# Kernel tuning notes

Measured on AMD Instinct MI355X. Metric: run time of the kernel, lower is better.

The kernel has to match this reference:

```python
import jax, jax.numpy as jnp
import numpy as np

N = 50000
E = 800000
HIGH, LOW, EMB = 128, 32, 64
HID, HEADS, OUT = 32, 8, 8
IN1 = HIGH + EMB  # 192
IN2 = HID * HEADS  # 256
NEG_SLOPE = 0.2


def setup_inputs() -> dict:
    key = jax.random.key(0)
    ks = jax.random.split(key, 12)
    s = lambda k, shape: (jax.random.normal(k, shape, dtype=jnp.float32) * 0.1)
    return {
        "high_dim_features": jax.random.normal(ks[0], (N, HIGH), dtype=jnp.float32),
        "low_dim_features": jax.random.normal(ks[1], (N, LOW), dtype=jnp.float32),
        "edge_index": jax.random.randint(ks[2], (2, E), 0, N, dtype=jnp.int32),
        "W_emb": s(ks[3], (LOW, EMB)),
        "b_emb": jnp.zeros((EMB,), jnp.float32),
        "W1": s(ks[4], (IN1, HEADS * HID)),
        "att_src1": s(ks[5], (HEADS, HID)),
        "att_dst1": s(ks[6], (HEADS, HID)),
        "b1": jnp.zeros((HEADS * HID,), jnp.float32),
        "W2": s(ks[7], (IN2, OUT)),
        "att_src2": s(ks[8], (1, OUT)),
        "att_dst2": s(ks[9], (1, OUT)),
        "b2": jnp.zeros((OUT,), jnp.float32),
    }


def _gat_layer(x, src, dst, W, att_src, att_dst, bias, heads, out_ch, concat):
    # x: [N, F_in]; src/dst: [E'] (self-loops already appended)
    n = x.shape[0]
    h = (x @ W).reshape(n, heads, out_ch)            # [N, H, C]
    a_src = jnp.einsum('nhc,hc->nh', h, att_src)     # [N, H]
    a_dst = jnp.einsum('nhc,hc->nh', h, att_dst)
    alpha = a_src[src] + a_dst[dst]                  # [E', H]
    alpha = jax.nn.leaky_relu(alpha, NEG_SLOPE)
    # segment softmax over incoming edges per destination node
    m = jax.ops.segment_max(alpha, dst, num_segments=n)
    ea = jnp.exp(alpha - m[dst])
    z = jax.ops.segment_sum(ea, dst, num_segments=n)
    alpha = ea / (z[dst] + 1e-16)                    # [E', H]
    msg = h[src] * alpha[:, :, None]                 # [E', H, C]
    out = jax.ops.segment_sum(msg, dst, num_segments=n)  # [N, H, C]
    if concat:
        out = out.reshape(n, heads * out_ch)
    else:
        out = out.mean(axis=1)
    return out + bias


def reference(high_dim_features, low_dim_features, edge_index,
              W_emb, b_emb, W1, att_src1, att_dst1, b1,
              W2, att_src2, att_dst2, b2):
    # embedding + elu, concat
    emb = jax.nn.elu(low_dim_features @ W_emb + b_emb)
    x = jnp.concatenate([high_dim_features, emb], axis=1)  # [N, IN1]
    # add self-loops (PyG default)
    loops = jnp.arange(N, dtype=edge_index.dtype)
    src = jnp.concatenate([edge_index[0], loops])
    dst = jnp.concatenate([edge_index[1], loops])
    x = _gat_layer(x, src, dst, W1, att_src1, att_dst1, b1, HEADS, HID, True)
    x = jax.nn.elu(x)  # dropout: eval mode no-op
    x = _gat_layer(x, src, dst, W2, att_src2, att_dst2, b2, 1, OUT, False)
    return jax.nn.log_softmax(x, axis=1)
```

## Files before the change

### kernel.cpp

```cpp
#include <hip/hip_runtime.h>
#include <hip/hip_bf16.h>

typedef __hip_bfloat16 bf16;
typedef short bf16x8 __attribute__((ext_vector_type(8)));
typedef float f32x4  __attribute__((ext_vector_type(4)));

#define CHK 8192

__device__ __forceinline__ float bf2f(bf16 v){ return __bfloat162float(v); }
__device__ __forceinline__ bf16  f2bf(float f){ return __float2bfloat16(f); }
__device__ __forceinline__ float lrelu(float a){ return a > 0.f ? a : 0.2f*a; }
__device__ __forceinline__ float bfbits(short s){
    union{unsigned u; float f;} cv; cv.u = ((unsigned)(unsigned short)s) << 16; return cv.f;
}
__device__ __forceinline__ short bf16s(float f){ bf16 q = f2bf(f); return *(short*)&q; }
__device__ __forceinline__ float cvtf(const void* p, int i, int isb){
    return isb ? bf2f(((const bf16*)p)[i]) : ((const float*)p)[i];
}
__device__ __forceinline__ short cvts(const void* p, int i, int isb){
    return isb ? ((const short*)p)[i] : bf16s(((const float*)p)[i]);
}
__device__ __forceinline__ bf16x8 load8(const void* base, size_t off, int isb){
    if (isb) return *(const bf16x8*)((const bf16*)base + off);
    const float* f = (const float*)base + off;
    f32x4 v0 = *(const f32x4*)f;
    f32x4 v1 = *(const f32x4*)(f + 4);
    short r[8];
    #pragma unroll
    for (int j = 0; j < 4; j++) r[j]   = bf16s(v0[j]);
    #pragma unroll
    for (int j = 0; j < 4; j++) r[4+j] = bf16s(v1[j]);
    return *(const bf16x8*)r;
}

__global__ __launch_bounds__(256) void k_init(const unsigned short* __restrict__ raw,
        int* __restrict__ flag, const int* __restrict__ dst,
        int* __restrict__ bucketCnt, int E, int NBUK, int nBlk){
    __shared__ int h[256];
    int t = threadIdx.x;
    if (blockIdx.x == 0){
        unsigned short w = raw[2*t];
        int e = (w >> 7) & 0xFF;
        int ok = (e >= 90 && e <= 140) ? 1 : 0;
        __shared__ int cnt;
        if (t == 0) cnt = 0;
        __syncthreads();
        atomicAdd(&cnt, ok);
        __syncthreads();
        if (t == 0) *flag = (cnt >= 192) ? 1 : 0;
    }
    h[t] = 0;
    __syncthreads();
    for (int i = blockIdx.x*256 + t; i < E; i += nBlk*256)
        atomicAdd(&h[((unsigned)dst[i]) >> 8], 1);
    __syncthreads();
    if (t < NBUK && h[t]) atomicAdd(&bucketCnt[t], h[t]);
}

__global__ __launch_bounds__(256) void k_prep(const void* __restrict__ low,
        const void* __restrict__ Wemb, const void* __restrict__ bemb,
        const void* __restrict__ W1, const void* __restrict__ W2,
        bf16* __restrict__ emb, bf16* __restrict__ Bp, bf16* __restrict__ Bp2,
        const int* __restrict__ flag, int N, int nEmb){
    __shared__ float wem[2048 + 64];
    __shared__ short lows[1024];
    int t = threadIdx.x;
    int b = blockIdx.x;
    int isb = *flag;
    if (b >= nEmb){
        int i = (b - nEmb)*256 + t;
        if (i < 16*6*64*8){
            int j = i & 7;
            int lane = (i >> 3) & 63;
            int r = i >> 9;
            int kt = r % 6, nt = r / 6;
            int k = kt*32 + (lane >> 4)*8 + j;
            int n = nt*16 + (lane & 15);
            *(short*)&Bp[i] = cvts(W1, k*256 + n, isb);
        } else {
            int i2 = i - 16*6*64*8;
            if (i2 >= 8*64*8) return;
            int j = i2 & 7;
            int lane = (i2 >> 3) & 63;
            int kt = i2 >> 9;
            int k = kt*32 + (lane >> 4)*8 + j;
            int n = lane & 15;
            *(short*)&Bp2[i2] = (n < 8) ? cvts(W2, k*8 + n, isb) : (short)0;
        }
        return;
    }
    int nb0 = b * 32;
    for (int i = t; i < 2048; i += 256) wem[i] = cvtf(Wemb, i, isb);
    if (t < 64) wem[2048 + t] = cvtf(bemb, t, isb);
    int lim = (N - nb0) * 32; if (lim > 1024) lim = 1024;
    for (int i = t; i < 1024; i += 256)
        lows[i] = (i < lim) ? cvts(low, nb0*32 + i, isb) : (short)0;
    __syncthreads();
    int nl = t >> 3, j8 = (t & 7) * 8;
    float acc[8];
    #pragma unroll
    for (int j = 0; j < 8; j++) acc[j] = wem[2048 + j8 + j];
    for (int k = 0; k < 32; k++){
        float lv = bfbits(lows[nl*32 + k]);
        f32x4 w0 = *(const f32x4*)&wem[k*64 + j8];
        f32x4 w1 = *(const f32x4*)&wem[k*64 + j8 + 4];
        #pragma unroll
        for (int j = 0; j < 4; j++) acc[j]   += lv * w0[j];
        #pragma unroll
        for (int j = 0; j < 4; j++) acc[4+j] += lv * w1[j];
    }
    int n = nb0 + nl;
    if (n < N){
        short ov[8];
        #pragma unroll
        for (int j = 0; j < 8; j++){
            float v = acc[j];
            ov[j] = bf16s(v > 0.f ? v : expm1f(v));
        }
        *(bf16x8*)&emb[(size_t)n*64 + j8] = *(const bf16x8*)ov;
    }
}

__global__ __launch_bounds__(256) void k_bscan(const int* __restrict__ bucketCnt,
        int* __restrict__ bucketPtr, int* __restrict__ bucketCur,
        int* __restrict__ rowptr, int N, int E, int NBUK){
    __shared__ int sd[256];
    int t = threadIdx.x;
    int v = (t < NBUK) ? bucketCnt[t] : 0;
    sd[t] = v;
    __syncthreads();
    #pragma unroll
    for (int off = 1; off < 256; off <<= 1){
        int a = (t >= off) ? sd[t - off] : 0;
        __syncthreads();
        sd[t] += a;
        __syncthreads();
    }
    int excl = sd[t] - v;
    if (t < NBUK){ bucketPtr[t] = excl; bucketCur[t] = excl; }
    if (t == 0){ bucketPtr[NBUK] = sd[255]; rowptr[N] = E + N; }
}

__global__ __launch_bounds__(256, 3) void k_sg(
        const int* __restrict__ ei, int* __restrict__ bucketCur, int* __restrict__ pk,
        const void* __restrict__ highv, const bf16* __restrict__ emb,
        const bf16* __restrict__ Bp, const void* __restrict__ attS,
        const void* __restrict__ attD, bf16* __restrict__ h1,
        float* __restrict__ a_s, float* __restrict__ a_d,
        const int* __restrict__ flag, int N, int E, int nG, int NBUK){
    const int RS = 260;
    __shared__ union SM {
        struct { float eb[16*260 + 16]; float att[512]; } g;
        struct { unsigned short dstS[CHK]; int hist[256]; int cur[256]; } s;
    } sm;
    int t = threadIdx.x;
    if ((int)blockIdx.x >= nG){
        int cb = blockIdx.x - nG;
        int base = cb * CHK;
        int cnt = E - base; if (cnt > CHK) cnt = CHK;
        sm.s.hist[t] = 0;
        __syncthreads();
        const int* dstp = ei + E + base;
        for (int i = t; i < cnt; i += 256){
            int d = dstp[i];
            sm.s.dstS[i] = (unsigned short)d;
            atomicAdd(&sm.s.hist[((unsigned)d) >> 8], 1);
        }
        __syncthreads();
        if (t < NBUK){
            int c = sm.s.hist[t];
            sm.s.cur[t] = c ? atomicAdd(&bucketCur[t], c) : 0;
        }
        __syncthreads();
        const int* srcp = ei + base;
        for (int i = t; i < cnt; i += 256){
            int d = sm.s.dstS[i];
            int pos = atomicAdd(&sm.s.cur[d >> 8], 1);
            pk[pos] = ((d & 255) << 24) | srcp[i];
        }
        return;
    }
    float* eb  = sm.g.eb;
    float* att = sm.g.att;
    int isb = *flag;
    att[t] = cvtf(attS, t, isb);
    att[256 + t] = cvtf(attD, t, isb);
    int w = t >> 6, lane = t & 63;
    int m_lo = lane & 15, quad = lane >> 4;
    int m0 = blockIdx.x * 64;
    int mr[4];
    #pragma unroll
    for (int rt = 0; rt < 4; rt++){
        int m = m0 + rt*16 + m_lo;
        mr[rt] = m < N ? m : N-1;
    }
    f32x4 acc[4][4];
    #pragma unroll
    for (int rt = 0; rt < 4; rt++)
        #pragma unroll
        for (int ct = 0; ct < 4; ct++) acc[rt][ct] = (f32x4){0.f,0.f,0.f,0.f};

    #pragma unroll 2
    for (int kt = 0; kt < 6; kt++){
        bf16x8 a[4], b[4];
        if (kt < 4){
            #pragma unroll
            for (int rt = 0; rt < 4; rt++)
                a[rt] = load8(highv, (size_t)mr[rt]*128 + kt*32 + quad*8, isb);
        } else {
            #pragma unroll
            for (int rt = 0; rt < 4; rt++)
                a[rt] = *(const bf16x8*)&emb[(size_t)mr[rt]*64 + (kt-4)*32 + quad*8];
        }
        #pragma unroll
        for (int ct = 0; ct < 4; ct++)
            b[ct] = *(const bf16x8*)&Bp[(size_t)(((w*4 + ct)*6 + kt)*64 + lane)*8];
        #pragma unroll
        for (int rt = 0; rt < 4; rt++)
            #pragma unroll
            for (int ct = 0; ct < 4; ct++)
                acc[rt][ct] = __builtin_amdgcn_mfma_f32_16x16x32_bf16(a[rt], b[ct], acc[rt][ct], 0, 0, 0);
    }

    #pragma unroll 1
    for (int rt = 0; rt < 4; rt++){
        __syncthreads();
        #pragma unroll
        for (int ct = 0; ct < 4; ct++)
            #pragma unroll
            for (int reg = 0; reg < 4; reg++)
                eb[(quad*4 + reg)*RS + w*64 + ct*16 + m_lo] = acc[rt][ct][reg];
        __syncthreads();
        int r = t >> 4, cb = t & 15;
        int c0 = cb * 16;
        int m = m0 + rt*16 + r;
        f32x4 v[4];
        #pragma unroll
        for (int p = 0; p < 4; p++) v[p] = *(const f32x4*)&eb[r*RS + c0 + p*4];
        float ps = 0.f, pd = 0.f;
        #pragma unroll
        for (int p = 0; p < 4; p++)
            #pragma unroll
            for (int j = 0; j < 4; j++){
                ps += v[p][j] * att[c0 + p*4 + j];
                pd += v[p][j] * att[256 + c0 + p*4 + j];
            }
        if (m < N){
            short ov[16];
            #pragma unroll
            for (int p = 0; p < 4; p++)
                #pragma unroll
                for (int j = 0; j < 4; j++) ov[p*4+j] = bf16s(v[p][j]);
            *(bf16x8*)&h1[(size_t)m*256 + c0]     = *(const bf16x8*)&ov[0];
            *(bf16x8*)&h1[(size_t)m*256 + c0 + 8] = *(const bf16x8*)&ov[8];
        }
        ps += __shfl_xor(ps, 1);
        pd += __shfl_xor(pd, 1);
        if (((t & 1) == 0) && m < N){
            int hd = cb >> 1;
            a_s[m*8 + hd] = ps;
            a_d[m*8 + hd] = pd;
        }
    }
}

__global__ __launch_bounds__(256) void k_fine(const int* __restrict__ bucketPtr,
        const int* __restrict__ pk, int* __restrict__ rowptr, int* __restrict__ srcs,
        int N){
    __shared__ int cnt[256];
    __shared__ int sd[256];
    int t = threadIdx.x;
    int b = blockIdx.x;
    int d0 = b << 8;
    int nd = N - d0; if (nd > 256) nd = 256;
    int ebeg = bucketPtr[b], eend = bucketPtr[b+1];
    cnt[t] = (t < nd) ? 1 : 0;
    __syncthreads();
    for (int i = ebeg + t; i < eend; i += 256)
        atomicAdd(&cnt[((unsigned)pk[i]) >> 24], 1);
    __syncthreads();
    int v = cnt[t];
    sd[t] = v;
    __syncthreads();
    #pragma unroll
    for (int off = 1; off < 256; off <<= 1){
        int a = (t >= off) ? sd[t - off] : 0;
        __syncthreads();
        sd[t] += a;
        __syncthreads();
    }
    int r = ebeg + d0 + sd[t] - v;
    if (t < nd){
        rowptr[d0 + t] = r;
        srcs[r] = d0 + t;
        cnt[t] = r + 1;
    }
    __syncthreads();
    for (int i = ebeg + t; i < eend; i += 256){
        int p = pk[i];
        int pos = atomicAdd(&cnt[((unsigned)p) >> 24], 1);
        srcs[pos] = p & 0xFFFFFF;
    }
}

__global__ __launch_bounds__(256) void k_edge1(const int* __restrict__ rowptr,
        const int* __restrict__ srcs, const float* __restrict__ a_s,
        const float* __restrict__ a_d, const bf16* __restrict__ h1,
        const void* __restrict__ b1, bf16* __restrict__ x2,
        const int* __restrict__ flag, int N){
    int t = threadIdx.x;
    int lane = t & 63, wv = t >> 6;
    int n = blockIdx.x*4 + wv;
    if (n >= N) return;
    int beg = rowptr[n];
    int deg = rowptr[n+1] - beg;

    int cl = lane & 31;
    int hb = cl >> 2;
    int half = lane >> 5;
    float adb = a_d[n*8 + hb];

    float acc[8];
    #pragma unroll
    for (int j = 0; j < 8; j++) acc[j] = 0.f;
    float z = 0.f;

    int e = half;
    for (; e + 6 < deg; e += 8){
        int s0 = srcs[beg + e];
        int s1 = srcs[beg + e + 2];
        int s2 = srcs[beg + e + 4];
        int s3 = srcs[beg + e + 6];
        float w0 = __expf(fminf(lrelu(a_s[s0*8 + hb] + adb), 80.f));
        float w1 = __expf(fminf(lrelu(a_s[s1*8 + hb] + adb), 80.f));
        float w2 = __expf(fminf(lrelu(a_s[s2*8 + hb] + adb), 80.f));
        float w3 = __expf(fminf(lrelu(a_s[s3*8 + hb] + adb), 80.f));
        bf16x8 v0 = *(const bf16x8*)&h1[(size_t)s0*256 + cl*8];
        bf16x8 v1 = *(const bf16x8*)&h1[(size_t)s1*256 + cl*8];
        bf16x8 v2 = *(const bf16x8*)&h1[(size_t)s2*256 + cl*8];
        bf16x8 v3 = *(const bf16x8*)&h1[(size_t)s3*256 + cl*8];
        z += (w0 + w1) + (w2 + w3);
        #pragma unroll
        for (int j = 0; j < 8; j++) acc[j] += w0 * bfbits(v0[j]);
        #pragma unroll
        for (int j = 0; j < 8; j++) acc[j] += w1 * bfbits(v1[j]);
        #pragma unroll
        for (int j = 0; j < 8; j++) acc[j] += w2 * bfbits(v2[j]);
        #pragma unroll
        for (int j = 0; j < 8; j++) acc[j] += w3 * bfbits(v3[j]);
    }
    for (; e < deg; e += 2){
        int s = srcs[beg + e];
        float w = __expf(fminf(lrelu(a_s[s*8 + hb] + adb), 80.f));
        bf16x8 hv = *(const bf16x8*)&h1[(size_t)s*256 + cl*8];
        z += w;
        #pragma unroll
        for (int j = 0; j < 8; j++) acc[j] += w * bfbits(hv[j]);
    }
    #pragma unroll
    for (int j = 0; j < 8; j++) acc[j] += __shfl_xor(acc[j], 32);
    z += __shfl_xor(z, 32);
    float rz = 1.f / (z + 1e-16f);

    if (half == 0){
        int isb = *flag;
        bf16x8 bv = load8(b1, cl*8, isb);
        short ov[8];
        #pragma unroll
        for (int j = 0; j < 8; j++){
            float v = acc[j] * rz + bfbits(bv[j]);
            ov[j] = bf16s(v > 0.f ? v : expm1f(v));
        }
        *(bf16x8*)&x2[(size_t)n*256 + cl*8] = *(const bf16x8*)ov;
    }
}

__global__ __launch_bounds__(256) void k_gemm2(const bf16* __restrict__ x2,
        const bf16* __restrict__ Bp2, const void* __restrict__ attS,
        const void* __restrict__ attD, float* __restrict__ h2,
        float* __restrict__ a2s, float* __restrict__ a2d,
        const int* __restrict__ flag, int N){
    int t = threadIdx.x;
    int isb = *flag;
    int w = t >> 6, lane = t & 63;
    int m_lo = lane & 15, quad = lane >> 4;
    int m0 = blockIdx.x*64 + w*16;
    int mr = m0 + m_lo; if (mr >= N) mr = N-1;
    f32x4 acc = (f32x4){0.f,0.f,0.f,0.f};
    #pragma unroll
    for (int kt = 0; kt < 8; kt++){
        bf16x8 a = *(const bf16x8*)&x2[(size_t)mr*256 + kt*32 + quad*8];
        bf16x8 b = *(const bf16x8*)&Bp2[(size_t)(kt*64 + lane)*8];
        acc = __builtin_amdgcn_mfma_f32_16x16x32_bf16(a, b, acc, 0, 0, 0);
    }
    float s2 = (m_lo < 8) ? cvtf(attS, m_lo, isb) : 0.f;
    float d2 = (m_lo < 8) ? cvtf(attD, m_lo, isb) : 0.f;
    #pragma unroll
    for (int reg = 0; reg < 4; reg++){
        int m = m0 + quad*4 + reg;
        float val = acc[reg];
        float ps = val * s2, pd = val * d2;
        ps += __shfl_xor(ps, 1); ps += __shfl_xor(ps, 2);
        ps += __shfl_xor(ps, 4); ps += __shfl_xor(ps, 8);
        pd += __shfl_xor(pd, 1); pd += __shfl_xor(pd, 2);
        pd += __shfl_xor(pd, 4); pd += __shfl_xor(pd, 8);
        if (m < N){
            if (m_lo < 8) h2[(size_t)m*8 + m_lo] = val;
            if (m_lo == 0){ a2s[m] = ps; a2d[m] = pd; }
        }
    }
}

__global__ __launch_bounds__(256) void k_edge2(const int* __restrict__ rowptr,
        const int* __restrict__ srcs, const float* __restrict__ a2s,
        const float* __restrict__ a2d, const float* __restrict__ h2,
        const void* __restrict__ b2, void* __restrict__ outv,
        const int* __restrict__ flag, int N){
    int t = threadIdx.x;
    int lane = t & 63, wv = t >> 6;
    int n = blockIdx.x*4 + wv;
    if (n >= N) return;
    int beg = rowptr[n];
    int deg = rowptr[n+1] - beg;
    float adh = a2d[n];
    int ep = lane >> 3, c = lane & 7;
    float acc = 0.f, z = 0.f;
    for (int e = ep; e < deg; e += 8){
        int s = srcs[beg + e];
        float w = __expf(fminf(lrelu(a2s[s] + adh), 80.f));
        z += w;
        acc += w * h2[(size_t)s*8 + c];
    }
    acc += __shfl_xor(acc, 8);
    acc += __shfl_xor(acc, 16);
    acc += __shfl_xor(acc, 32);
    z += __shfl_xor(z, 8);
    z += __shfl_xor(z, 16);
    z += __shfl_xor(z, 32);
    int isb = *flag;
    float val = acc / (z + 1e-16f) + cvtf(b2, c, isb);
    float mx = val;
    mx = fmaxf(mx, __shfl_xor(mx, 1));
    mx = fmaxf(mx, __shfl_xor(mx, 2));
    mx = fmaxf(mx, __shfl_xor(mx, 4));
    float se = __expf(val - mx);
    se += __shfl_xor(se, 1); se += __shfl_xor(se, 2); se += __shfl_xor(se, 4);
    float r = val - mx - __logf(se);
    if (lane < 8){
        if (isb) ((bf16*)outv)[(size_t)n*8 + c] = f2bf(r);
        else     ((float*)outv)[(size_t)n*8 + c] = r;
    }
}

extern "C" void kernel_launch(void* const* d_in, const int* in_sizes, int n_in,
                              void* d_out, int out_size, void* d_ws, size_t ws_size,
                              hipStream_t stream) {
    const int* ei = (const int*)d_in[2];
    const int N = in_sizes[0] / 128;
    const int E = in_sizes[2] / 2;
    const int ET = E + N;
    const int NBUK = (N + 255) >> 8;

    char* p = (char*)d_ws;
    auto alloc = [&](size_t bytes) -> void* {
        char* r = p;
        p += (bytes + 255) & ~(size_t)255;
        return (void*)r;
    };
    int*   flag      = (int*)  alloc(256);
    int*   bucketCnt = (int*)  alloc((size_t)NBUK*4);
    int*   bucketPtr = (int*)  alloc((size_t)(NBUK+1)*4);
    int*   bucketCur = (int*)  alloc((size_t)NBUK*4);
    int*   rowptr    = (int*)  alloc((size_t)(N+1)*4);
    int*   srcs      = (int*)  alloc((size_t)ET*4);
    int*   pk        = (int*)  alloc((size_t)E*4);
    bf16*  Bp        = (bf16*) alloc((size_t)192*256*2);
    bf16*  Bp2       = (bf16*) alloc((size_t)8*64*8*2);
    bf16*  emb       = (bf16*) alloc((size_t)N*64*2);
    bf16*  h1        = (bf16*) alloc((size_t)N*256*2);
    float* a_s       = (float*)alloc((size_t)N*8*4);
    float* a_d       = (float*)alloc((size_t)N*8*4);
    bf16*  x2        = (bf16*) alloc((size_t)N*256*2);
    float* h2        = (float*)alloc((size_t)N*8*4);
    float* a2s       = (float*)alloc((size_t)N*4);
    float* a2d       = (float*)alloc((size_t)N*4);

    hipMemsetAsync(bucketCnt, 0, (size_t)NBUK*4, stream);
    k_init<<<256, 256, 0, stream>>>((const unsigned short*)d_in[0], flag,
            ei + E, bucketCnt, E, NBUK, 256);
    {
        int nEmb  = (N + 31)/32;
        int nPack = (16*6*64*8 + 8*64*8 + 255)/256;
        k_prep<<<nEmb + nPack, 256, 0, stream>>>(d_in[1], d_in[3], d_in[4],
                d_in[5], d_in[9], emb, Bp, Bp2, flag, N, nEmb);
    }
    k_bscan<<<1, 256, 0, stream>>>(bucketCnt, bucketPtr, bucketCur, rowptr, N, E, NBUK);
    {
        int nG = (N + 63)/64;
        int nScat = (E + CHK - 1)/CHK;
        k_sg<<<nG + nScat, 256, 0, stream>>>(ei, bucketCur, pk,
                d_in[0], emb, Bp, d_in[6], d_in[7], h1, a_s, a_d, flag, N, E, nG, NBUK);
    }
    k_fine<<<NBUK, 256, 0, stream>>>(bucketPtr, pk, rowptr, srcs, N);
    k_edge1<<<(N + 3)/4, 256, 0, stream>>>(rowptr, srcs, a_s, a_d, h1, d_in[8], x2, flag, N);
    k_gemm2<<<(N + 63)/64, 256, 0, stream>>>(x2, Bp2, d_in[10], d_in[11], h2, a2s, a2d, flag, N);
    k_edge2<<<(N + 3)/4, 256, 0, stream>>>(rowptr, srcs, a2s, a2d, h2, d_in[12], d_out, flag, N);
}
```

Baseline: 313.4 us.

## Use per-wave histograms in edge bucketing and pad global bucket cursors

The edge scatter and fine-sort kernels now give each wavefront its own contiguous slice and its own LDS histogram and cursor arrays, which cuts LDS atomic contention and keeps writes from a wave contiguous. The global bucket cursors are padded to one per 64 bytes, scatter blocks are placed before the GEMM blocks in the grid, the scatter chunk size shrinks so more blocks run, and each embedding block now handles four 32-node tiles so the weight table is loaded into LDS less often. The costs are more global cursor atomics from the larger number of chunks and extra shared memory.

New measurement: 315.6 us. About the same (+0.7%).

```diff
diff --git a/kernel.cpp b/kernel.cpp
--- a/kernel.cpp
+++ b/kernel.cpp
@@ -5,7 +5,7 @@
 typedef short bf16x8 __attribute__((ext_vector_type(8)));
 typedef float f32x4  __attribute__((ext_vector_type(4)));
 
-#define CHK 8192
+#define CHK 2048
 
 __device__ __forceinline__ float bf2f(bf16 v){ return __bfloat162float(v); }
 __device__ __forceinline__ bf16  f2bf(float f){ return __float2bfloat16(f); }
@@ -89,35 +89,40 @@
         }
         return;
     }
-    int nb0 = b * 32;
     for (int i = t; i < 2048; i += 256) wem[i] = cvtf(Wemb, i, isb);
     if (t < 64) wem[2048 + t] = cvtf(bemb, t, isb);
-    int lim = (N - nb0) * 32; if (lim > 1024) lim = 1024;
-    for (int i = t; i < 1024; i += 256)
-        lows[i] = (i < lim) ? cvts(low, nb0*32 + i, isb) : (short)0;
-    __syncthreads();
     int nl = t >> 3, j8 = (t & 7) * 8;
-    float acc[8];
-    #pragma unroll
-    for (int j = 0; j < 8; j++) acc[j] = wem[2048 + j8 + j];
-    for (int k = 0; k < 32; k++){
-        float lv = bfbits(lows[nl*32 + k]);
-        f32x4 w0 = *(const f32x4*)&wem[k*64 + j8];
-        f32x4 w1 = *(const f32x4*)&wem[k*64 + j8 + 4];
-        #pragma unroll
-        for (int j = 0; j < 4; j++) acc[j]   += lv * w0[j];
-        #pragma unroll
-        for (int j = 0; j < 4; j++) acc[4+j] += lv * w1[j];
-    }
-    int n = nb0 + nl;
-    if (n < N){
-        short ov[8];
-        #pragma unroll
-        for (int j = 0; j < 8; j++){
-            float v = acc[j];
-            ov[j] = bf16s(v > 0.f ? v : expm1f(v));
-        }
-        *(bf16x8*)&emb[(size_t)n*64 + j8] = *(const bf16x8*)ov;
+    for (int tile = 0; tile < 4; tile++){
+        int nb0 = b*128 + tile*32;
+        __syncthreads();
+        int lim = (N - nb0) * 32;
+        if (lim > 1024) lim = 1024;
+        if (lim < 0) lim = 0;
+        for (int i = t; i < 1024; i += 256)
+            lows[i] = (i < lim) ? cvts(low, nb0*32 + i, isb) : (short)0;
+        __syncthreads();
+        float acc[8];
+        #pragma unroll
+        for (int j = 0; j < 8; j++) acc[j] = wem[2048 + j8 + j];
+        for (int k = 0; k < 32; k++){
+            float lv = bfbits(lows[nl*32 + k]);
+            f32x4 w0 = *(const f32x4*)&wem[k*64 + j8];
+            f32x4 w1 = *(const f32x4*)&wem[k*64 + j8 + 4];
+            #pragma unroll
+            for (int j = 0; j < 4; j++) acc[j]   += lv * w0[j];
+            #pragma unroll
+            for (int j = 0; j < 4; j++) acc[4+j] += lv * w1[j];
+        }
+        int n = nb0 + nl;
+        if (n < N){
+            short ov[8];
+            #pragma unroll
+            for (int j = 0; j < 8; j++){
+                float v = acc[j];
+                ov[j] = bf16s(v > 0.f ? v : expm1f(v));
+            }
+            *(bf16x8*)&emb[(size_t)n*64 + j8] = *(const bf16x8*)ov;
+        }
     }
 }
 
@@ -137,7 +142,7 @@
         __syncthreads();
     }
     int excl = sd[t] - v;
-    if (t < NBUK){ bucketPtr[t] = excl; bucketCur[t] = excl; }
+    if (t < NBUK){ bucketPtr[t] = excl; bucketCur[t*16] = excl; }
     if (t == 0){ bucketPtr[NBUK] = sd[255]; rowptr[N] = E + N; }
 }
 
@@ -147,35 +152,46 @@
         const bf16* __restrict__ Bp, const void* __restrict__ attS,
         const void* __restrict__ attD, bf16* __restrict__ h1,
         float* __restrict__ a_s, float* __restrict__ a_d,
-        const int* __restrict__ flag, int N, int E, int nG, int NBUK){
+        const int* __restrict__ flag, int N, int E, int nScat, int NBUK){
     const int RS = 260;
     __shared__ union SM {
         struct { float eb[16*260 + 16]; float att[512]; } g;
-        struct { unsigned short dstS[CHK]; int hist[256]; int cur[256]; } s;
+        struct { unsigned short dstS[CHK]; int hist[4][256]; int cur[4][256]; } s;
     } sm;
     int t = threadIdx.x;
-    if ((int)blockIdx.x >= nG){
-        int cb = blockIdx.x - nG;
-        int base = cb * CHK;
+    if ((int)blockIdx.x < nScat){
+        int base = blockIdx.x * CHK;
         int cnt = E - base; if (cnt > CHK) cnt = CHK;
-        sm.s.hist[t] = 0;
+        int wv = t >> 6, lane = t & 63;
+        #pragma unroll
+        for (int w = 0; w < 4; w++) sm.s.hist[w][t] = 0;
         __syncthreads();
         const int* dstp = ei + E + base;
-        for (int i = t; i < cnt; i += 256){
+        const int* srcp = ei + base;
+        int per = (cnt + 3) >> 2;
+        int wb = wv*per, we = wb + per;
+        if (we > cnt) we = cnt;
+        if (wb > cnt) wb = cnt;
+        for (int i = wb + lane; i < we; i += 64){
             int d = dstp[i];
             sm.s.dstS[i] = (unsigned short)d;
-            atomicAdd(&sm.s.hist[((unsigned)d) >> 8], 1);
+            atomicAdd(&sm.s.hist[wv][((unsigned)d) >> 8], 1);
         }
         __syncthreads();
         if (t < NBUK){
-            int c = sm.s.hist[t];
-            sm.s.cur[t] = c ? atomicAdd(&bucketCur[t], c) : 0;
-        }
-        __syncthreads();
-        const int* srcp = ei + base;
-        for (int i = t; i < cnt; i += 256){
+            int h0 = sm.s.hist[0][t], h1v = sm.s.hist[1][t];
+            int h2 = sm.s.hist[2][t], h3 = sm.s.hist[3][t];
+            int c = h0 + h1v + h2 + h3;
+            int bs = c ? atomicAdd(&bucketCur[t*16], c) : 0;
+            sm.s.cur[0][t] = bs;
+            sm.s.cur[1][t] = bs + h0;
+            sm.s.cur[2][t] = bs + h0 + h1v;
+            sm.s.cur[3][t] = bs + h0 + h1v + h2;
+        }
+        __syncthreads();
+        for (int i = wb + lane; i < we; i += 64){
             int d = sm.s.dstS[i];
-            int pos = atomicAdd(&sm.s.cur[d >> 8], 1);
+            int pos = atomicAdd(&sm.s.cur[wv][d >> 8], 1);
             pk[pos] = ((d & 255) << 24) | srcp[i];
         }
         return;
@@ -187,7 +203,7 @@
     att[256 + t] = cvtf(attD, t, isb);
     int w = t >> 6, lane = t & 63;
     int m_lo = lane & 15, quad = lane >> 4;
-    int m0 = blockIdx.x * 64;
+    int m0 = (blockIdx.x - nScat) * 64;
     int mr[4];
     #pragma unroll
     for (int rt = 0; rt < 4; rt++){
@@ -267,19 +283,29 @@
 __global__ __launch_bounds__(256) void k_fine(const int* __restrict__ bucketPtr,
         const int* __restrict__ pk, int* __restrict__ rowptr, int* __restrict__ srcs,
         int N){
-    __shared__ int cnt[256];
+    __shared__ int hist[4][256];
+    __shared__ int cur[4][256];
     __shared__ int sd[256];
     int t = threadIdx.x;
+    int wv = t >> 6, lane = t & 63;
     int b = blockIdx.x;
     int d0 = b << 8;
-    int nd = N - d0; if (nd > 256) nd = 256;
+    int nd = N - d0; if (nd > 256) nd = 256; if (nd < 0) nd = 0;
     int ebeg = bucketPtr[b], eend = bucketPtr[b+1];
-    cnt[t] = (t < nd) ? 1 : 0;
-    __syncthreads();
-    for (int i = ebeg + t; i < eend; i += 256)
-        atomicAdd(&cnt[((unsigned)pk[i]) >> 24], 1);
-    __syncthreads();
-    int v = cnt[t];
+    int tot = eend - ebeg;
+    int per = (tot + 3) >> 2;
+    int wb = wv*per, we = wb + per;
+    if (we > tot) we = tot;
+    if (wb > tot) wb = tot;
+    #pragma unroll
+    for (int w = 0; w < 4; w++) hist[w][t] = 0;
+    __syncthreads();
+    for (int i = wb + lane; i < we; i += 64)
+        atomicAdd(&hist[wv][((unsigned)pk[ebeg + i]) >> 24], 1);
+    __syncthreads();
+    int h0 = hist[0][t], h1 = hist[1][t], h2 = hist[2][t], h3 = hist[3][t];
+    int selfc = (t < nd) ? 1 : 0;
+    int v = selfc + h0 + h1 + h2 + h3;
     sd[t] = v;
     __syncthreads();
     #pragma unroll
@@ -293,12 +319,16 @@
     if (t < nd){
         rowptr[d0 + t] = r;
         srcs[r] = d0 + t;
-        cnt[t] = r + 1;
-    }
-    __syncthreads();
-    for (int i = ebeg + t; i < eend; i += 256){
-        int p = pk[i];
-        int pos = atomicAdd(&cnt[((unsigned)p) >> 24], 1);
+    }
+    int c0 = r + selfc;
+    cur[0][t] = c0;
+    cur[1][t] = c0 + h0;
+    cur[2][t] = c0 + h0 + h1;
+    cur[3][t] = c0 + h0 + h1 + h2;
+    __syncthreads();
+    for (int i = wb + lane; i < we; i += 64){
+        int p = pk[ebeg + i];
+        int pos = atomicAdd(&cur[wv][((unsigned)p) >> 24], 1);
         srcs[pos] = p & 0xFFFFFF;
     }
 }
@@ -470,7 +500,7 @@
     int*   flag      = (int*)  alloc(256);
     int*   bucketCnt = (int*)  alloc((size_t)NBUK*4);
     int*   bucketPtr = (int*)  alloc((size_t)(NBUK+1)*4);
-    int*   bucketCur = (int*)  alloc((size_t)NBUK*4);
+    int*   bucketCur = (int*)  alloc((size_t)NBUK*16*4);
     int*   rowptr    = (int*)  alloc((size_t)(N+1)*4);
     int*   srcs      = (int*)  alloc((size_t)ET*4);
     int*   pk        = (int*)  alloc((size_t)E*4);
@@ -489,7 +519,7 @@
     k_init<<<256, 256, 0, stream>>>((const unsigned short*)d_in[0], flag,
             ei + E, bucketCnt, E, NBUK, 256);
     {
-        int nEmb  = (N + 31)/32;
+        int nEmb  = (N + 127)/128;
         int nPack = (16*6*64*8 + 8*64*8 + 255)/256;
         k_prep<<<nEmb + nPack, 256, 0, stream>>>(d_in[1], d_in[3], d_in[4],
                 d_in[5], d_in[9], emb, Bp, Bp2, flag, N, nEmb);
@@ -498,8 +528,8 @@
     {
         int nG = (N + 63)/64;
         int nScat = (E + CHK - 1)/CHK;
-        k_sg<<<nG + nScat, 256, 0, stream>>>(ei, bucketCur, pk,
-                d_in[0], emb, Bp, d_in[6], d_in[7], h1, a_s, a_d, flag, N, E, nG, NBUK);
+        k_sg<<<nScat + nG, 256, 0, stream>>>(ei, bucketCur, pk,
+                d_in[0], emb, Bp, d_in[6], d_in[7], h1, a_s, a_d, flag, N, E, nScat, NBUK);
     }
     k_fine<<<NBUK, 256, 0, stream>>>(bucketPtr, pk, rowptr, srcs, N);
     k_edge1<<<(N + 3)/4, 256, 0, stream>>>(rowptr, srcs, a_s, a_d, h1, d_in[8], x2, flag, N);
```
